# Performance work log

Hardware: AMD Instinct MI355X
Metric: run time of the kernel (lower is better)

Reference implementation:

```python
import jax, jax.numpy as jnp
import numpy as np

DIM = 384
NUM_HEADS = 12
DILATIONS = (1, 2, 3)
KSZ = 3
B, N = 4, 8192
HEAD_DIM = DIM // NUM_HEADS          # 32
ND = len(DILATIONS)                  # num_dilation
CD = DIM // ND                       # channels per dilation group
SCALE = HEAD_DIM ** -0.5


def setup_inputs() -> dict:
    key = jax.random.key(0)
    k0, k1, k2 = jax.random.split(key, 3)
    s = 0.02
    return {
        "x": jax.random.normal(k0, (B, N, DIM), dtype=jnp.float32),
        "Wqkv": jax.random.normal(k1, (3 * DIM, DIM), dtype=jnp.float32) * s,
        "bqkv": jnp.zeros((3 * DIM,), dtype=jnp.float32),
        "Wproj": jax.random.normal(k2, (DIM, DIM), dtype=jnp.float32) * s,
        "bproj": jnp.zeros((DIM,), dtype=jnp.float32),
    }


def _unfold_seq(t, dil, ksz):
    # Faithful nn.Unfold(ksz, dilation=dil, padding=dil*(ksz-1)//2) applied to
    # t viewed as (B, C, N, 1): of the ksz*ksz taps, only the center-width
    # column is in-bounds; the rest are zero padding. Tap order is (kh, kw)
    # with kw fastest, matching torch's unfold channel layout.
    # t: (B, nh, hd, N) -> (B, nh, hd, ksz*ksz, N)
    _, _, _, n = t.shape
    pad = dil * (ksz - 1) // 2
    tp = jnp.pad(t, ((0, 0), (0, 0), (0, 0), (pad, pad)))
    zeros = jnp.zeros_like(t)
    taps = []
    for kh in range(ksz):
        row = jax.lax.dynamic_slice_in_dim(tp, kh * dil, n, axis=3)
        for kw in range(ksz):
            taps.append(row if kw == ksz // 2 else zeros)
    return jnp.stack(taps, axis=3)


def _dilate_attn(q, k, v, dil):
    # q,k,v: (B, CD, N) -> (B, N, CD)
    b, cd, n = q.shape
    nh = cd // HEAD_DIM
    q = q.reshape(b, nh, HEAD_DIM, n)
    k = _unfold_seq(k.reshape(b, nh, HEAD_DIM, n), dil, KSZ)   # (b,nh,hd,k2,n)
    v = _unfold_seq(v.reshape(b, nh, HEAD_DIM, n), dil, KSZ)
    attn = jax.nn.softmax(jnp.einsum("bhdn,bhdjn->bhnj", q, k) * SCALE, axis=-1)
    out = jnp.einsum("bhnj,bhdjn->bhnd", attn, v)              # (b,nh,n,hd)
    return out.transpose(0, 2, 1, 3).reshape(b, n, cd)


def reference(x, Wqkv, bqkv, Wproj, bproj):
    b, n, c = x.shape
    # (b,n,3c) -> (nd, 3, b, cd, n), matching torch permute(3,2,0,4,1)
    qkv = (x @ Wqkv.T + bqkv).reshape(b, n, 3, ND, CD).transpose(3, 2, 0, 4, 1)
    outs = [_dilate_attn(qkv[i, 0], qkv[i, 1], qkv[i, 2], DILATIONS[i]) for i in range(ND)]
    xo = jnp.stack(outs, axis=2).reshape(b, n, c)  # (b,n,nd,cd) -> (b,n,c)
    return xo @ Wproj.T + bproj
```

## Files before the change

### kernel.cpp

```cpp
#include <hip/hip_runtime.h>

#define DIM     384
#define QKV_CH  1152
#define HD      32
#define CD      128
#define BATCH   4
#define SEQ     8192
#define ROWS    (BATCH*SEQ)
#define SCALE   0.17677669529663687f

#define KB8         48
#define FRAG_STRIDE (KB8*128)
#define XRB_MAX     (ROWS/16 - 1)
#define LSTR        136

typedef short bf16x8 __attribute__((ext_vector_type(8)));
typedef float f32x4  __attribute__((ext_vector_type(4)));

__device__ __forceinline__ unsigned short f2bf(float f) {
  unsigned int u = __float_as_uint(f);
  u += 0x7fffu + ((u >> 16) & 1u);
  return (unsigned short)(u >> 16);
}
__device__ __forceinline__ float bf2f(unsigned short b) {
  return __uint_as_float(((unsigned int)b) << 16);
}
__device__ __forceinline__ void unpack4(uint2 u, float* f) {
  f[0] = bf2f((unsigned short)(u.x & 0xffffu)); f[1] = bf2f((unsigned short)(u.x >> 16));
  f[2] = bf2f((unsigned short)(u.y & 0xffffu)); f[3] = bf2f((unsigned short)(u.y >> 16));
}


template<int K>
__global__ __launch_bounds__(256) void cvt_swz(const float* __restrict__ in,
                                               unsigned short* __restrict__ out) {
  const int KB = K / 8;
  int cid = blockIdx.x * 256 + threadIdx.x;
  int rl = cid & 15;
  int q  = cid >> 4;
  int rb = q / KB;
  int kb = q - rb * KB;
  const float* p = in + (size_t)(rb * 16 + rl) * K + kb * 8;
  float4 a = *(const float4*)p;
  float4 b = *(const float4*)(p + 4);
  unsigned int w0 = (unsigned int)f2bf(a.x) | ((unsigned int)f2bf(a.y) << 16);
  unsigned int w1 = (unsigned int)f2bf(a.z) | ((unsigned int)f2bf(a.w) << 16);
  unsigned int w2 = (unsigned int)f2bf(b.x) | ((unsigned int)f2bf(b.y) << 16);
  unsigned int w3 = (unsigned int)f2bf(b.z) | ((unsigned int)f2bf(b.w) << 16);
  uint4 u; u.x = w0; u.y = w1; u.z = w2; u.w = w3;
  *(uint4*)(out + (size_t)cid * 8) = u;
}

template<int OUT_BF16, int K, int NT>
__global__ __launch_bounds__(256) void gemm_swz(const unsigned short* __restrict__ A,
                                                const unsigned short* __restrict__ Bt,
                                                const float* __restrict__ bias,
                                                void* __restrict__ Cv) {
  const int KB = K / 8;
  const int t = threadIdx.x;
  const int wave = t >> 6, lane = t & 63;
  const int quad = lane >> 4, l16 = lane & 15;
  const int row0 = blockIdx.x * 128, col0 = blockIdx.y * 128;
  const int wm = (wave & 1) * 64, wn = (wave >> 1) * 64;

  const unsigned short* PA[4];
  const unsigned short* PB[4];
#pragma unroll
  for (int mi = 0; mi < 4; ++mi)
    PA[mi] = A + (size_t)(((row0 + wm) >> 4) + mi) * KB * 128 + lane * 8;
#pragma unroll
  for (int ni = 0; ni < 4; ++ni)
    PB[ni] = Bt + (size_t)(((col0 + wn) >> 4) + ni) * KB * 128 + lane * 8;

  f32x4 acc[4][4] = {};

#pragma unroll
  for (int kk = 0; kk < K / 32; ++kk) {
    bf16x8 af[4], bfv[4];
#pragma unroll
    for (int mi = 0; mi < 4; ++mi) af[mi]  = *(const bf16x8*)(PA[mi] + kk * 512);
#pragma unroll
    for (int ni = 0; ni < 4; ++ni) bfv[ni] = *(const bf16x8*)(PB[ni] + kk * 512);
#pragma unroll
    for (int mi = 0; mi < 4; ++mi)
#pragma unroll
      for (int ni = 0; ni < 4; ++ni)
        acc[mi][ni] = __builtin_amdgcn_mfma_f32_16x16x32_bf16(bfv[ni], af[mi], acc[mi][ni], 0, 0, 0);
  }

  float4 bv[4];
#pragma unroll
  for (int ni = 0; ni < 4; ++ni)
    bv[ni] = *(const float4*)&bias[col0 + wn + ni * 16 + quad * 4];

#pragma unroll
  for (int mi = 0; mi < 4; ++mi) {
    size_t gr = (size_t)(row0 + wm + mi * 16 + l16);
#pragma unroll
    for (int ni = 0; ni < 4; ++ni) {
      int gc = col0 + wn + ni * 16 + quad * 4;
      float v0 = acc[mi][ni][0] + bv[ni].x;
      float v1 = acc[mi][ni][1] + bv[ni].y;
      float v2 = acc[mi][ni][2] + bv[ni].z;
      float v3 = acc[mi][ni][3] + bv[ni].w;
      if (OUT_BF16) {
        uint2 u;
        u.x = (unsigned int)f2bf(v0) | ((unsigned int)f2bf(v1) << 16);
        u.y = (unsigned int)f2bf(v2) | ((unsigned int)f2bf(v3) << 16);
        *(uint2*)&((unsigned short*)Cv)[gr * NT + gc] = u;
      } else {
        float4 o; o.x = v0; o.y = v1; o.z = v2; o.w = v3;
        *(float4*)&((float*)Cv)[gr * NT + gc] = o;
      }
    }
  }
}

__global__ __launch_bounds__(256, 2) void fused_qkv_attn(
    const unsigned short* __restrict__ X,
    const unsigned short* __restrict__ W,
    const float* __restrict__ bqkv,
    unsigned short* __restrict__ out) {
  __shared__ unsigned short sm[34816];
  unsigned short* q_t = sm;
  unsigned short* k_t = sm + 64 * LSTR;
  unsigned short* v_t = sm + 160 * LSTR;

  const int t = threadIdx.x;
  const int w = t >> 6, lane = t & 63;
  const int quad = lane >> 4, l16 = lane & 15;
  const int d = blockIdx.y;
  const int row0 = blockIdx.x * 64;
  const int rb0 = row0 >> 4;

  const unsigned short* pa[6];
#pragma unroll
  for (int j = 0; j < 6; ++j) {
    int xrb = rb0 - 1 + j;
    xrb = xrb < 0 ? 0 : (xrb > XRB_MAX ? XRB_MAX : xrb);
    pa[j] = X + (size_t)xrb * FRAG_STRIDE + lane * 8;
  }
  const unsigned short *pbq[2], *pbk[2], *pbv[2];
#pragma unroll
  for (int c = 0; c < 2; ++c) {
    int wrb = d * 8 + w * 2 + c;
    pbq[c] = W + (size_t)wrb * FRAG_STRIDE + lane * 8;
    pbk[c] = W + (size_t)(wrb + 24) * FRAG_STRIDE + lane * 8;
    pbv[c] = W + (size_t)(wrb + 48) * FRAG_STRIDE + lane * 8;
  }

  f32x4 aq[4][2] = {}, ak[6][2] = {}, av[6][2] = {};

#pragma unroll
  for (int kk = 0; kk < 12; ++kk) {
    bf16x8 a[6];
#pragma unroll
    for (int j = 0; j < 6; ++j) a[j] = *(const bf16x8*)(pa[j] + kk * 512);
    bf16x8 bq[2], bk[2], bv[2];
#pragma unroll
    for (int c = 0; c < 2; ++c) {
      bq[c] = *(const bf16x8*)(pbq[c] + kk * 512);
      bk[c] = *(const bf16x8*)(pbk[c] + kk * 512);
      bv[c] = *(const bf16x8*)(pbv[c] + kk * 512);
    }
#pragma unroll
    for (int c = 0; c < 2; ++c) {
#pragma unroll
      for (int j = 0; j < 4; ++j)
        aq[j][c] = __builtin_amdgcn_mfma_f32_16x16x32_bf16(bq[c], a[j + 1], aq[j][c], 0, 0, 0);
#pragma unroll
      for (int j = 0; j < 6; ++j)
        ak[j][c] = __builtin_amdgcn_mfma_f32_16x16x32_bf16(bk[c], a[j], ak[j][c], 0, 0, 0);
#pragma unroll
      for (int j = 0; j < 6; ++j)
        av[j][c] = __builtin_amdgcn_mfma_f32_16x16x32_bf16(bv[c], a[j], av[j][c], 0, 0, 0);
    }
  }

#pragma unroll
  for (int c = 0; c < 2; ++c) {
    int colb = w * 32 + c * 16 + quad * 4;
    float4 b_q = *(const float4*)&bqkv[d * CD + colb];
    float4 b_k = *(const float4*)&bqkv[384 + d * CD + colb];
    float4 b_v = *(const float4*)&bqkv[768 + d * CD + colb];
#pragma unroll
    for (int j = 0; j < 4; ++j) {
      uint2 u;
      u.x = (unsigned int)f2bf(aq[j][c][0] + b_q.x) | ((unsigned int)f2bf(aq[j][c][1] + b_q.y) << 16);
      u.y = (unsigned int)f2bf(aq[j][c][2] + b_q.z) | ((unsigned int)f2bf(aq[j][c][3] + b_q.w) << 16);
      *(uint2*)&q_t[(j * 16 + l16) * LSTR + colb] = u;
    }
#pragma unroll
    for (int j = 0; j < 6; ++j) {
      uint2 u;
      u.x = (unsigned int)f2bf(ak[j][c][0] + b_k.x) | ((unsigned int)f2bf(ak[j][c][1] + b_k.y) << 16);
      u.y = (unsigned int)f2bf(ak[j][c][2] + b_k.z) | ((unsigned int)f2bf(ak[j][c][3] + b_k.w) << 16);
      *(uint2*)&k_t[(j * 16 + l16) * LSTR + colb] = u;
    }
#pragma unroll
    for (int j = 0; j < 6; ++j) {
      uint2 u;
      u.x = (unsigned int)f2bf(av[j][c][0] + b_v.x) | ((unsigned int)f2bf(av[j][c][1] + b_v.y) << 16);
      u.y = (unsigned int)f2bf(av[j][c][2] + b_v.z) | ((unsigned int)f2bf(av[j][c][3] + b_v.w) << 16);
      *(uint2*)&v_t[(j * 16 + l16) * LSTR + colb] = u;
    }
  }
  __syncthreads();

  const int h = t >> 6;
  const int r = t & 63;
  const int dil = d + 1;
  const int n = (row0 + r) & (SEQ - 1);

  float q[32];
  {
    const uint2* qp = (const uint2*)&q_t[r * LSTR + h * HD];
#pragma unroll
    for (int c = 0; c < 8; ++c) unpack4(qp[c], &q[c * 4]);
  }

  float ex[3];
  int   valid[3];
#pragma unroll
  for (int kh = 0; kh < 3; ++kh) {
    int off = (kh - 1) * dil;
    int nn = n + off;
    int v = (nn >= 0) && (nn < SEQ);
    valid[kh] = v;
    float l = 0.f;
    if (v) {
      const uint2* kp = (const uint2*)&k_t[(r + 16 + off) * LSTR + h * HD];
#pragma unroll
      for (int c = 0; c < 8; ++c) {
        float kkv[4]; unpack4(kp[c], kkv);
#pragma unroll
        for (int j = 0; j < 4; ++j) l += q[c * 4 + j] * kkv[j];
      }
    }
    ex[kh] = v ? __expf(l * SCALE) : 1.f;
  }
  float inv = 1.f / (ex[0] + ex[1] + ex[2] + 6.f);

  float o[32];
#pragma unroll
  for (int e = 0; e < 32; ++e) o[e] = 0.f;
#pragma unroll
  for (int kh = 0; kh < 3; ++kh) {
    if (!valid[kh]) continue;
    int off = (kh - 1) * dil;
    const uint2* vp = (const uint2*)&v_t[(r + 16 + off) * LSTR + h * HD];
    float wgt = ex[kh];
#pragma unroll
    for (int c = 0; c < 8; ++c) {
      float vv[4]; unpack4(vp[c], vv);
#pragma unroll
      for (int j = 0; j < 4; ++j) o[c * 4 + j] += wgt * vv[j];
    }
  }

  int row = row0 + r;
  int ch0 = d * CD + h * HD;
  unsigned short* op = out + ((size_t)(row >> 4) * KB8 + (ch0 >> 3)) * 128 + (row & 15) * 8;
#pragma unroll
  for (int c = 0; c < 4; ++c) {
    uint4 u;
    u.x = (unsigned int)f2bf(o[c*8+0] * inv) | ((unsigned int)f2bf(o[c*8+1] * inv) << 16);
    u.y = (unsigned int)f2bf(o[c*8+2] * inv) | ((unsigned int)f2bf(o[c*8+3] * inv) << 16);
    u.z = (unsigned int)f2bf(o[c*8+4] * inv) | ((unsigned int)f2bf(o[c*8+5] * inv) << 16);
    u.w = (unsigned int)f2bf(o[c*8+6] * inv) | ((unsigned int)f2bf(o[c*8+7] * inv) << 16);
    *(uint4*)(op + c * 128) = u;
  }
}

extern "C" void kernel_launch(void* const* d_in, const int* in_sizes, int n_in,
                              void* d_out, int out_size, void* d_ws, size_t ws_size,
                              hipStream_t stream) {
  const float* x     = (const float*)d_in[0];
  const float* Wqkv  = (const float*)d_in[1];
  const float* bqkv  = (const float*)d_in[2];
  const float* Wproj = (const float*)d_in[3];
  const float* bproj = (const float*)d_in[4];
  float* out = (float*)d_out;

  char* ws = (char*)d_ws;
  unsigned short* x_swz     = (unsigned short*)(ws);
  unsigned short* attn_swz  = (unsigned short*)(ws + 25165824);
  unsigned short* wqkv_swz  = (unsigned short*)(ws + 50331648);
  unsigned short* wproj_swz = (unsigned short*)(ws + 51216384);

  cvt_swz<DIM><<<ROWS * (DIM / 8) / 256, 256, 0, stream>>>(x, x_swz);
  cvt_swz<DIM><<<QKV_CH * (DIM / 8) / 256, 256, 0, stream>>>(Wqkv, wqkv_swz);
  cvt_swz<DIM><<<DIM * (DIM / 8) / 256, 256, 0, stream>>>(Wproj, wproj_swz);

  fused_qkv_attn<<<dim3(ROWS / 64, 3), 256, 0, stream>>>(x_swz, wqkv_swz, bqkv, attn_swz);

  gemm_swz<0, DIM, DIM><<<dim3(ROWS / 128, DIM / 128), 256, 0, stream>>>(
      attn_swz, wproj_swz, bproj, (void*)out);
}
```

Measured before the change: 170.2 us.

## Fuse QKV projection, dilated attention, and output projection into one kernel

Merges the QKV+attention kernel and the output projection GEMM into a single kernel. Each block of 64 rows loops over the three dilation groups and accumulates the projection output in registers, so the bf16 attention intermediate no longer makes a round trip through global memory. The LDS layout also changes to swizzled 16x8 fragments so the attention output can feed MFMA directly. In exchange, the grid shrinks to one third of its previous size, each block runs the three groups serially with extra barriers, the X fragments are reloaded per group, and the running projection sum is kept in packed bf16, which adds rounding error.

```diff
diff --git a/kernel.cpp b/kernel.cpp
--- a/kernel.cpp
+++ b/kernel.cpp
@@ -8,11 +8,8 @@
 #define SEQ     8192
 #define ROWS    (BATCH*SEQ)
 #define SCALE   0.17677669529663687f
-
-#define KB8         48
-#define FRAG_STRIDE (KB8*128)
-#define XRB_MAX     (ROWS/16 - 1)
-#define LSTR        136
+#define FRAG_STRIDE 6144
+#define XRB_MAX (ROWS/16 - 1)
 
 typedef short bf16x8 __attribute__((ext_vector_type(8)));
 typedef float f32x4  __attribute__((ext_vector_type(4)));
@@ -25,9 +22,14 @@
 __device__ __forceinline__ float bf2f(unsigned short b) {
   return __uint_as_float(((unsigned int)b) << 16);
 }
-__device__ __forceinline__ void unpack4(uint2 u, float* f) {
-  f[0] = bf2f((unsigned short)(u.x & 0xffffu)); f[1] = bf2f((unsigned short)(u.x >> 16));
-  f[2] = bf2f((unsigned short)(u.y & 0xffffu)); f[3] = bf2f((unsigned short)(u.y >> 16));
+__device__ __forceinline__ float bflo(unsigned int u) { return bf2f((unsigned short)(u & 0xffffu)); }
+__device__ __forceinline__ float bfhi(unsigned int u) { return bf2f((unsigned short)(u >> 16)); }
+__device__ __forceinline__ unsigned int pack2(float a, float b) {
+  return (unsigned int)f2bf(a) | ((unsigned int)f2bf(b) << 16);
+}
+__device__ __forceinline__ void unpack8(uint4 u, float* f) {
+  f[0] = bflo(u.x); f[1] = bfhi(u.x); f[2] = bflo(u.y); f[3] = bfhi(u.y);
+  f[4] = bflo(u.z); f[5] = bfhi(u.z); f[6] = bflo(u.w); f[7] = bfhi(u.w);
 }
 
 
@@ -43,93 +45,26 @@
   const float* p = in + (size_t)(rb * 16 + rl) * K + kb * 8;
   float4 a = *(const float4*)p;
   float4 b = *(const float4*)(p + 4);
-  unsigned int w0 = (unsigned int)f2bf(a.x) | ((unsigned int)f2bf(a.y) << 16);
-  unsigned int w1 = (unsigned int)f2bf(a.z) | ((unsigned int)f2bf(a.w) << 16);
-  unsigned int w2 = (unsigned int)f2bf(b.x) | ((unsigned int)f2bf(b.y) << 16);
-  unsigned int w3 = (unsigned int)f2bf(b.z) | ((unsigned int)f2bf(b.w) << 16);
-  uint4 u; u.x = w0; u.y = w1; u.z = w2; u.w = w3;
+  uint4 u;
+  u.x = pack2(a.x, a.y); u.y = pack2(a.z, a.w);
+  u.z = pack2(b.x, b.y); u.w = pack2(b.z, b.w);
   *(uint4*)(out + (size_t)cid * 8) = u;
 }
 
-template<int OUT_BF16, int K, int NT>
-__global__ __launch_bounds__(256) void gemm_swz(const unsigned short* __restrict__ A,
-                                                const unsigned short* __restrict__ Bt,
-                                                const float* __restrict__ bias,
-                                                void* __restrict__ Cv) {
-  const int KB = K / 8;
-  const int t = threadIdx.x;
-  const int wave = t >> 6, lane = t & 63;
-  const int quad = lane >> 4, l16 = lane & 15;
-  const int row0 = blockIdx.x * 128, col0 = blockIdx.y * 128;
-  const int wm = (wave & 1) * 64, wn = (wave >> 1) * 64;
-
-  const unsigned short* PA[4];
-  const unsigned short* PB[4];
-#pragma unroll
-  for (int mi = 0; mi < 4; ++mi)
-    PA[mi] = A + (size_t)(((row0 + wm) >> 4) + mi) * KB * 128 + lane * 8;
-#pragma unroll
-  for (int ni = 0; ni < 4; ++ni)
-    PB[ni] = Bt + (size_t)(((col0 + wn) >> 4) + ni) * KB * 128 + lane * 8;
-
-  f32x4 acc[4][4] = {};
-
-#pragma unroll
-  for (int kk = 0; kk < K / 32; ++kk) {
-    bf16x8 af[4], bfv[4];
-#pragma unroll
-    for (int mi = 0; mi < 4; ++mi) af[mi]  = *(const bf16x8*)(PA[mi] + kk * 512);
-#pragma unroll
-    for (int ni = 0; ni < 4; ++ni) bfv[ni] = *(const bf16x8*)(PB[ni] + kk * 512);
-#pragma unroll
-    for (int mi = 0; mi < 4; ++mi)
-#pragma unroll
-      for (int ni = 0; ni < 4; ++ni)
-        acc[mi][ni] = __builtin_amdgcn_mfma_f32_16x16x32_bf16(bfv[ni], af[mi], acc[mi][ni], 0, 0, 0);
-  }
-
-  float4 bv[4];
-#pragma unroll
-  for (int ni = 0; ni < 4; ++ni)
-    bv[ni] = *(const float4*)&bias[col0 + wn + ni * 16 + quad * 4];
-
-#pragma unroll
-  for (int mi = 0; mi < 4; ++mi) {
-    size_t gr = (size_t)(row0 + wm + mi * 16 + l16);
-#pragma unroll
-    for (int ni = 0; ni < 4; ++ni) {
-      int gc = col0 + wn + ni * 16 + quad * 4;
-      float v0 = acc[mi][ni][0] + bv[ni].x;
-      float v1 = acc[mi][ni][1] + bv[ni].y;
-      float v2 = acc[mi][ni][2] + bv[ni].z;
-      float v3 = acc[mi][ni][3] + bv[ni].w;
-      if (OUT_BF16) {
-        uint2 u;
-        u.x = (unsigned int)f2bf(v0) | ((unsigned int)f2bf(v1) << 16);
-        u.y = (unsigned int)f2bf(v2) | ((unsigned int)f2bf(v3) << 16);
-        *(uint2*)&((unsigned short*)Cv)[gr * NT + gc] = u;
-      } else {
-        float4 o; o.x = v0; o.y = v1; o.z = v2; o.w = v3;
-        *(float4*)&((float*)Cv)[gr * NT + gc] = o;
-      }
-    }
-  }
-}
-
-__global__ __launch_bounds__(256, 2) void fused_qkv_attn(
+__global__ __launch_bounds__(256, 2) void mega_kernel(
     const unsigned short* __restrict__ X,
-    const unsigned short* __restrict__ W,
+    const unsigned short* __restrict__ Wq,
     const float* __restrict__ bqkv,
-    unsigned short* __restrict__ out) {
-  __shared__ unsigned short sm[34816];
-  unsigned short* q_t = sm;
-  unsigned short* k_t = sm + 64 * LSTR;
-  unsigned short* v_t = sm + 160 * LSTR;
+    const unsigned short* __restrict__ Wp,
+    const float* __restrict__ bproj,
+    float* __restrict__ out) {
+  __shared__ unsigned short q_t[8192];
+  __shared__ unsigned short k_t[12288];
+  __shared__ unsigned short v_t[12288];
 
   const int t = threadIdx.x;
   const int w = t >> 6, lane = t & 63;
   const int quad = lane >> 4, l16 = lane & 15;
-  const int d = blockIdx.y;
   const int row0 = blockIdx.x * 64;
   const int rb0 = row0 >> 4;
 
@@ -140,135 +75,217 @@
     xrb = xrb < 0 ? 0 : (xrb > XRB_MAX ? XRB_MAX : xrb);
     pa[j] = X + (size_t)xrb * FRAG_STRIDE + lane * 8;
   }
-  const unsigned short *pbq[2], *pbk[2], *pbv[2];
-#pragma unroll
-  for (int c = 0; c < 2; ++c) {
-    int wrb = d * 8 + w * 2 + c;
-    pbq[c] = W + (size_t)wrb * FRAG_STRIDE + lane * 8;
-    pbk[c] = W + (size_t)(wrb + 24) * FRAG_STRIDE + lane * 8;
-    pbv[c] = W + (size_t)(wrb + 48) * FRAG_STRIDE + lane * 8;
+
+  unsigned int run[4][6][2];
+#pragma unroll
+  for (int j = 0; j < 4; ++j)
+#pragma unroll
+    for (int i = 0; i < 6; ++i) { run[j][i][0] = 0u; run[j][i][1] = 0u; }
+
+
+#pragma unroll 1
+  for (int d = 0; d < 3; ++d) {
+    {
+      const unsigned short *pbq[2], *pbk[2];
+#pragma unroll
+      for (int c = 0; c < 2; ++c) {
+        int wrb = d * 8 + w * 2 + c;
+        pbq[c] = Wq + (size_t)wrb * FRAG_STRIDE + lane * 8;
+        pbk[c] = Wq + (size_t)(wrb + 24) * FRAG_STRIDE + lane * 8;
+      }
+      f32x4 aq[4][2] = {}, ak[6][2] = {};
+#pragma unroll
+      for (int kk = 0; kk < 12; ++kk) {
+        bf16x8 a[6];
+#pragma unroll
+        for (int j = 0; j < 6; ++j) a[j] = *(const bf16x8*)(pa[j] + kk * 512);
+        bf16x8 bq[2], bk[2];
+#pragma unroll
+        for (int c = 0; c < 2; ++c) {
+          bq[c] = *(const bf16x8*)(pbq[c] + kk * 512);
+          bk[c] = *(const bf16x8*)(pbk[c] + kk * 512);
+        }
+#pragma unroll
+        for (int c = 0; c < 2; ++c) {
+#pragma unroll
+          for (int j = 0; j < 4; ++j)
+            aq[j][c] = __builtin_amdgcn_mfma_f32_16x16x32_bf16(bq[c], a[j + 1], aq[j][c], 0, 0, 0);
+#pragma unroll
+          for (int j = 0; j < 6; ++j)
+            ak[j][c] = __builtin_amdgcn_mfma_f32_16x16x32_bf16(bk[c], a[j], ak[j][c], 0, 0, 0);
+        }
+      }
+#pragma unroll
+      for (int c = 0; c < 2; ++c) {
+        int colb = w * 32 + c * 16 + quad * 4;
+        int cblk = (colb >> 3);
+        int sub  = (colb & 7);
+        float4 b_q = *(const float4*)&bqkv[d * CD + colb];
+        float4 b_k = *(const float4*)&bqkv[384 + d * CD + colb];
+#pragma unroll
+        for (int j = 0; j < 4; ++j) {
+          uint2 u;
+          u.x = pack2(aq[j][c][0] + b_q.x, aq[j][c][1] + b_q.y);
+          u.y = pack2(aq[j][c][2] + b_q.z, aq[j][c][3] + b_q.w);
+          *(uint2*)&q_t[(j * 16 + cblk) * 128 + l16 * 8 + sub] = u;
+        }
+#pragma unroll
+        for (int j = 0; j < 6; ++j) {
+          uint2 u;
+          u.x = pack2(ak[j][c][0] + b_k.x, ak[j][c][1] + b_k.y);
+          u.y = pack2(ak[j][c][2] + b_k.z, ak[j][c][3] + b_k.w);
+          *(uint2*)&k_t[(j * 16 + cblk) * 128 + l16 * 8 + sub] = u;
+        }
+      }
+    }
+    {
+      const unsigned short* pbv[2];
+#pragma unroll
+      for (int c = 0; c < 2; ++c)
+        pbv[c] = Wq + (size_t)(d * 8 + w * 2 + c + 48) * FRAG_STRIDE + lane * 8;
+      f32x4 av[6][2] = {};
+#pragma unroll
+      for (int kk = 0; kk < 12; ++kk) {
+        bf16x8 a[6];
+#pragma unroll
+        for (int j = 0; j < 6; ++j) a[j] = *(const bf16x8*)(pa[j] + kk * 512);
+        bf16x8 bv[2];
+#pragma unroll
+        for (int c = 0; c < 2; ++c) bv[c] = *(const bf16x8*)(pbv[c] + kk * 512);
+#pragma unroll
+        for (int c = 0; c < 2; ++c)
+#pragma unroll
+          for (int j = 0; j < 6; ++j)
+            av[j][c] = __builtin_amdgcn_mfma_f32_16x16x32_bf16(bv[c], a[j], av[j][c], 0, 0, 0);
+      }
+#pragma unroll
+      for (int c = 0; c < 2; ++c) {
+        int colb = w * 32 + c * 16 + quad * 4;
+        int cblk = (colb >> 3), sub = (colb & 7);
+        float4 b_v = *(const float4*)&bqkv[768 + d * CD + colb];
+#pragma unroll
+        for (int j = 0; j < 6; ++j) {
+          uint2 u;
+          u.x = pack2(av[j][c][0] + b_v.x, av[j][c][1] + b_v.y);
+          u.y = pack2(av[j][c][2] + b_v.z, av[j][c][3] + b_v.w);
+          *(uint2*)&v_t[(j * 16 + cblk) * 128 + l16 * 8 + sub] = u;
+        }
+      }
+    }
+    __syncthreads();
+
+    {
+      const int h = w;
+      const int r = lane;
+      const int dil = d + 1;
+      const int n = (row0 + r) & (SEQ - 1);
+
+      float q[32];
+#pragma unroll
+      for (int c8 = 0; c8 < 4; ++c8) {
+        uint4 u = *(const uint4*)&q_t[((r >> 4) * 16 + h * 4 + c8) * 128 + (r & 15) * 8];
+        unpack8(u, &q[c8 * 8]);
+      }
+      __syncthreads();
+
+      float ex[3];
+      int   valid[3];
+#pragma unroll
+      for (int kh = 0; kh < 3; ++kh) {
+        int off = (kh - 1) * dil;
+        int nn = n + off;
+        int v = (nn >= 0) && (nn < SEQ);
+        valid[kh] = v;
+        float l = 0.f;
+        if (v) {
+          int rl = r + 16 + off;
+#pragma unroll
+          for (int c8 = 0; c8 < 4; ++c8) {
+            uint4 u = *(const uint4*)&k_t[((rl >> 4) * 16 + h * 4 + c8) * 128 + (rl & 15) * 8];
+            float kkv[8]; unpack8(u, kkv);
+#pragma unroll
+            for (int j = 0; j < 8; ++j) l += q[c8 * 8 + j] * kkv[j];
+          }
+        }
+        ex[kh] = v ? __expf(l * SCALE) : 1.f;
+      }
+      float inv = 1.f / (ex[0] + ex[1] + ex[2] + 6.f);
+
+      float o[32];
+#pragma unroll
+      for (int e = 0; e < 32; ++e) o[e] = 0.f;
+#pragma unroll
+      for (int kh = 0; kh < 3; ++kh) {
+        if (!valid[kh]) continue;
+        int off = (kh - 1) * dil;
+        int rl = r + 16 + off;
+        float wgt = ex[kh];
+#pragma unroll
+        for (int c8 = 0; c8 < 4; ++c8) {
+          uint4 u = *(const uint4*)&v_t[((rl >> 4) * 16 + h * 4 + c8) * 128 + (rl & 15) * 8];
+          float vv[8]; unpack8(u, vv);
+#pragma unroll
+          for (int j = 0; j < 8; ++j) o[c8 * 8 + j] += wgt * vv[j];
+        }
+      }
+#pragma unroll
+      for (int c8 = 0; c8 < 4; ++c8) {
+        uint4 u;
+        u.x = pack2(o[c8*8+0] * inv, o[c8*8+1] * inv);
+        u.y = pack2(o[c8*8+2] * inv, o[c8*8+3] * inv);
+        u.z = pack2(o[c8*8+4] * inv, o[c8*8+5] * inv);
+        u.w = pack2(o[c8*8+6] * inv, o[c8*8+7] * inv);
+        *(uint4*)&q_t[((r >> 4) * 16 + h * 4 + c8) * 128 + (r & 15) * 8] = u;
+      }
+    }
+    __syncthreads();
+
+    {
+      f32x4 p[4][6] = {};
+#pragma unroll
+      for (int kk = 0; kk < 4; ++kk) {
+        bf16x8 af[4];
+#pragma unroll
+        for (int j = 0; j < 4; ++j)
+          af[j] = *(const bf16x8*)&q_t[j * 2048 + kk * 512 + lane * 8];
+#pragma unroll
+        for (int i = 0; i < 6; ++i) {
+          bf16x8 bf = *(const bf16x8*)(Wp + (size_t)(w * 6 + i) * FRAG_STRIDE
+                                          + (d * 16 + kk * 4) * 128 + lane * 8);
+#pragma unroll
+          for (int j = 0; j < 4; ++j)
+            p[j][i] = __builtin_amdgcn_mfma_f32_16x16x32_bf16(bf, af[j], p[j][i], 0, 0, 0);
+        }
+      }
+#pragma unroll
+      for (int j = 0; j < 4; ++j)
+#pragma unroll
+        for (int i = 0; i < 6; ++i) {
+          float s0 = bflo(run[j][i][0]) + p[j][i][0];
+          float s1 = bfhi(run[j][i][0]) + p[j][i][1];
+          float s2 = bflo(run[j][i][1]) + p[j][i][2];
+          float s3 = bfhi(run[j][i][1]) + p[j][i][3];
+          run[j][i][0] = pack2(s0, s1);
+          run[j][i][1] = pack2(s2, s3);
+        }
+    }
+    __syncthreads();
   }
 
-  f32x4 aq[4][2] = {}, ak[6][2] = {}, av[6][2] = {};
-
-#pragma unroll
-  for (int kk = 0; kk < 12; ++kk) {
-    bf16x8 a[6];
-#pragma unroll
-    for (int j = 0; j < 6; ++j) a[j] = *(const bf16x8*)(pa[j] + kk * 512);
-    bf16x8 bq[2], bk[2], bv[2];
-#pragma unroll
-    for (int c = 0; c < 2; ++c) {
-      bq[c] = *(const bf16x8*)(pbq[c] + kk * 512);
-      bk[c] = *(const bf16x8*)(pbk[c] + kk * 512);
-      bv[c] = *(const bf16x8*)(pbv[c] + kk * 512);
-    }
-#pragma unroll
-    for (int c = 0; c < 2; ++c) {
-#pragma unroll
-      for (int j = 0; j < 4; ++j)
-        aq[j][c] = __builtin_amdgcn_mfma_f32_16x16x32_bf16(bq[c], a[j + 1], aq[j][c], 0, 0, 0);
-#pragma unroll
-      for (int j = 0; j < 6; ++j)
-        ak[j][c] = __builtin_amdgcn_mfma_f32_16x16x32_bf16(bk[c], a[j], ak[j][c], 0, 0, 0);
-#pragma unroll
-      for (int j = 0; j < 6; ++j)
-        av[j][c] = __builtin_amdgcn_mfma_f32_16x16x32_bf16(bv[c], a[j], av[j][c], 0, 0, 0);
-    }
-  }
-
-#pragma unroll
-  for (int c = 0; c < 2; ++c) {
-    int colb = w * 32 + c * 16 + quad * 4;
-    float4 b_q = *(const float4*)&bqkv[d * CD + colb];
-    float4 b_k = *(const float4*)&bqkv[384 + d * CD + colb];
-    float4 b_v = *(const float4*)&bqkv[768 + d * CD + colb];
-#pragma unroll
-    for (int j = 0; j < 4; ++j) {
-      uint2 u;
-      u.x = (unsigned int)f2bf(aq[j][c][0] + b_q.x) | ((unsigned int)f2bf(aq[j][c][1] + b_q.y) << 16);
-      u.y = (unsigned int)f2bf(aq[j][c][2] + b_q.z) | ((unsigned int)f2bf(aq[j][c][3] + b_q.w) << 16);
-      *(uint2*)&q_t[(j * 16 + l16) * LSTR + colb] = u;
-    }
-#pragma unroll
-    for (int j = 0; j < 6; ++j) {
-      uint2 u;
-      u.x = (unsigned int)f2bf(ak[j][c][0] + b_k.x) | ((unsigned int)f2bf(ak[j][c][1] + b_k.y) << 16);
-      u.y = (unsigned int)f2bf(ak[j][c][2] + b_k.z) | ((unsigned int)f2bf(ak[j][c][3] + b_k.w) << 16);
-      *(uint2*)&k_t[(j * 16 + l16) * LSTR + colb] = u;
-    }
-#pragma unroll
-    for (int j = 0; j < 6; ++j) {
-      uint2 u;
-      u.x = (unsigned int)f2bf(av[j][c][0] + b_v.x) | ((unsigned int)f2bf(av[j][c][1] + b_v.y) << 16);
-      u.y = (unsigned int)f2bf(av[j][c][2] + b_v.z) | ((unsigned int)f2bf(av[j][c][3] + b_v.w) << 16);
-      *(uint2*)&v_t[(j * 16 + l16) * LSTR + colb] = u;
-    }
-  }
-  __syncthreads();
-
-  const int h = t >> 6;
-  const int r = t & 63;
-  const int dil = d + 1;
-  const int n = (row0 + r) & (SEQ - 1);
-
-  float q[32];
-  {
-    const uint2* qp = (const uint2*)&q_t[r * LSTR + h * HD];
-#pragma unroll
-    for (int c = 0; c < 8; ++c) unpack4(qp[c], &q[c * 4]);
-  }
-
-  float ex[3];
-  int   valid[3];
-#pragma unroll
-  for (int kh = 0; kh < 3; ++kh) {
-    int off = (kh - 1) * dil;
-    int nn = n + off;
-    int v = (nn >= 0) && (nn < SEQ);
-    valid[kh] = v;
-    float l = 0.f;
-    if (v) {
-      const uint2* kp = (const uint2*)&k_t[(r + 16 + off) * LSTR + h * HD];
-#pragma unroll
-      for (int c = 0; c < 8; ++c) {
-        float kkv[4]; unpack4(kp[c], kkv);
-#pragma unroll
-        for (int j = 0; j < 4; ++j) l += q[c * 4 + j] * kkv[j];
-      }
-    }
-    ex[kh] = v ? __expf(l * SCALE) : 1.f;
-  }
-  float inv = 1.f / (ex[0] + ex[1] + ex[2] + 6.f);
-
-  float o[32];
-#pragma unroll
-  for (int e = 0; e < 32; ++e) o[e] = 0.f;
-#pragma unroll
-  for (int kh = 0; kh < 3; ++kh) {
-    if (!valid[kh]) continue;
-    int off = (kh - 1) * dil;
-    const uint2* vp = (const uint2*)&v_t[(r + 16 + off) * LSTR + h * HD];
-    float wgt = ex[kh];
-#pragma unroll
-    for (int c = 0; c < 8; ++c) {
-      float vv[4]; unpack4(vp[c], vv);
-#pragma unroll
-      for (int j = 0; j < 4; ++j) o[c * 4 + j] += wgt * vv[j];
-    }
-  }
-
-  int row = row0 + r;
-  int ch0 = d * CD + h * HD;
-  unsigned short* op = out + ((size_t)(row >> 4) * KB8 + (ch0 >> 3)) * 128 + (row & 15) * 8;
-#pragma unroll
-  for (int c = 0; c < 4; ++c) {
-    uint4 u;
-    u.x = (unsigned int)f2bf(o[c*8+0] * inv) | ((unsigned int)f2bf(o[c*8+1] * inv) << 16);
-    u.y = (unsigned int)f2bf(o[c*8+2] * inv) | ((unsigned int)f2bf(o[c*8+3] * inv) << 16);
-    u.z = (unsigned int)f2bf(o[c*8+4] * inv) | ((unsigned int)f2bf(o[c*8+5] * inv) << 16);
-    u.w = (unsigned int)f2bf(o[c*8+6] * inv) | ((unsigned int)f2bf(o[c*8+7] * inv) << 16);
-    *(uint4*)(op + c * 128) = u;
+#pragma unroll
+  for (int j = 0; j < 4; ++j) {
+    size_t gr = (size_t)(row0 + j * 16 + l16);
+#pragma unroll
+    for (int i = 0; i < 6; ++i) {
+      int gc = (w * 6 + i) * 16 + quad * 4;
+      float4 b = *(const float4*)&bproj[gc];
+      float4 o;
+      o.x = bflo(run[j][i][0]) + b.x;
+      o.y = bfhi(run[j][i][0]) + b.y;
+      o.z = bflo(run[j][i][1]) + b.z;
+      o.w = bfhi(run[j][i][1]) + b.w;
+      *(float4*)&out[gr * DIM + gc] = o;
+    }
   }
 }
 
@@ -284,16 +301,13 @@
 
   char* ws = (char*)d_ws;
   unsigned short* x_swz     = (unsigned short*)(ws);
-  unsigned short* attn_swz  = (unsigned short*)(ws + 25165824);
-  unsigned short* wqkv_swz  = (unsigned short*)(ws + 50331648);
-  unsigned short* wproj_swz = (unsigned short*)(ws + 51216384);
+  unsigned short* wqkv_swz  = (unsigned short*)(ws + 25165824);
+  unsigned short* wproj_swz = (unsigned short*)(ws + 26050560);
 
   cvt_swz<DIM><<<ROWS * (DIM / 8) / 256, 256, 0, stream>>>(x, x_swz);
   cvt_swz<DIM><<<QKV_CH * (DIM / 8) / 256, 256, 0, stream>>>(Wqkv, wqkv_swz);
   cvt_swz<DIM><<<DIM * (DIM / 8) / 256, 256, 0, stream>>>(Wproj, wproj_swz);
 
-  fused_qkv_attn<<<dim3(ROWS / 64, 3), 256, 0, stream>>>(x_swz, wqkv_swz, bqkv, attn_swz);
-
-  gemm_swz<0, DIM, DIM><<<dim3(ROWS / 128, DIM / 128), 256, 0, stream>>>(
-      attn_swz, wproj_swz, bproj, (void*)out);
-}
+  mega_kernel<<<ROWS / 64, 256, 0, stream>>>(x_swz, wqkv_swz, bqkv,
+                                             wproj_swz, bproj, out);
+}
```

Result: slower. 331.2 us (+94.6%).
